# Optimization experiments

Hardware: AMD Instinct MI355X
Metric: run time of the kernel (lower is better)

Reference implementation:

```python
import jax, jax.numpy as jnp
import numpy as np

B, L, D = 8, 2048, 64   # batch, length, input_dim
K, NU = 40, 32          # num scales, reservoir units
LEAKY = 0.0
REG = 1.0


def setup_inputs() -> dict:
    key = jax.random.key(0)
    k1, k2 = jax.random.split(key)
    x = jax.random.normal(k1, (B, L, D), dtype=jnp.float32)
    radii = jax.random.uniform(k2, (K,), dtype=jnp.float32, minval=0.1, maxval=0.99)
    rng = np.random.default_rng(0)
    W_in = jnp.asarray(rng.standard_normal((D, NU)).astype(np.float32))
    # uni_res=True: one sparse reservoir, spectral-radius normalized, repeated K times
    connectivity = min(1.0, 10.0 / NU)
    w = rng.standard_normal((NU, NU)) * (rng.random((NU, NU)) < connectivity)
    w = w / np.max(np.abs(np.linalg.eigvals(w)))
    W_res = jnp.asarray(np.repeat(w[None].astype(np.float32), K, axis=0))
    return {"x": x, "radii": radii, "W_in": W_in, "W_res": W_res}


def reference(x, radii, W_in, W_res):
    Bb, Ll, Dd = x.shape
    k, nu = W_res.shape[0], W_res.shape[1]
    T = Ll - 1
    xt = x @ W_in                                # [B,L,nu]
    Wr = W_res * radii[:, None, None]            # [k,nu,nu]
    ar = jnp.arange(k)

    # Multi-scale recurrence: scale r reads its own state delayed by r+1 steps.
    # Rolling buffer buf[:, r, j] holds column (t-1-j) of scale r's history, so
    # h_pre for scale r is the diagonal buf[:, r, r] (== h_history[:, r, t-r-1];
    # zero for t-r-1 < 0, matching the torch code's untouched zero init).
    def step(buf, x_t):                          # buf [B,k,k,nu], x_t [B,nu]
        h_pre = buf[:, ar, ar, :]                # [B,k,nu] diagonal gather
        h_t = x_t[:, None, :] + jnp.einsum('brn,rnm->brm', h_pre, Wr)
        new = LEAKY * h_pre + (1.0 - LEAKY) * jnp.tanh(h_t)
        buf = jnp.concatenate([new[:, :, None, :], buf[:, :, :-1, :]], axis=2)
        return buf, new

    buf0 = jnp.zeros((Bb, k, k, nu), x.dtype)
    _, hist = jax.lax.scan(step, buf0, jnp.swapaxes(xt[:, :T], 0, 1))
    h_hist = jnp.transpose(hist, (1, 2, 0, 3))   # [B,k,T,nu]

    # Scale i has L-1-i valid timesteps; mask instead of ragged slicing.
    t_idx = jnp.arange(T)
    mask = (t_idx[None, :] < (Ll - 1 - ar)[:, None]).astype(x.dtype)  # [k,T]
    Hm = h_hist * mask[None, :, :, None]          # [B,k,T,nu]
    idx = jnp.minimum(t_idx[None, :] + ar[:, None] + 1, Ll - 1)       # [k,T]
    Xm = x[:, idx, :] * mask[None, :, :, None]    # [B,k,T,D] (x shifted by i+1)

    eye = REG * jnp.eye(nu, dtype=x.dtype)
    HtH = jnp.einsum('bktn,bktm->bknm', Hm, Hm) + eye   # [B,k,nu,nu]
    HtX = jnp.einsum('bktn,bktd->bknd', Hm, Xm)         # [B,k,nu,D]
    W_out = jnp.linalg.solve(HtH, HtX)                  # [B,k,nu,D]

    err = jnp.einsum('bktn,bknd->bktd', Hm, W_out) - Xm
    f_norms = jnp.sum(err, axis=(0, 2, 3))              # [k]
    features = W_out.reshape(Bb, k, nu * Dd)            # [B,k,nu*D]
    return features, f_norms
```

## Files before the change

kernel.cpp:

```cpp
#include <hip/hip_runtime.h>

#define B_ 8
#define L_ 2048
#define D_ 64
#define K_ 40
#define NU_ 32
#define T_ 2047
#define NSPLIT 8

#define XT_OFF   0
#define XT_SZ    (B_*L_*NU_)
#define HH_OFF   (XT_OFF + XT_SZ)
#define HH_SZ    (B_*K_*T_*NU_)
#define HTHP_OFF (HH_OFF + HH_SZ)
#define HTHP_SZ  (NSPLIT*B_*K_*NU_*NU_)
#define HTXP_OFF (HTHP_OFF + HTHP_SZ)
#define HTXP_SZ  (NSPLIT*B_*K_*NU_*D_)
#define SH_OFF   (HTXP_OFF + HTXP_SZ)
#define SH_SZ    (B_*K_*NU_)
#define SX_OFF   (SH_OFF + SH_SZ)
#define SX_SZ    (B_*K_)

#if __has_builtin(__builtin_amdgcn_exp2f)
#define EXP2F(x) __builtin_amdgcn_exp2f(x)
#else
#define EXP2F(x) __expf((x)*0.6931471805599453f)
#endif
#if __has_builtin(__builtin_amdgcn_rcpf)
#define RCPF(x) __builtin_amdgcn_rcpf(x)
#else
#define RCPF(x) (1.0f/(x))
#endif

__global__ __launch_bounds__(256) void k1_xt(const float* __restrict__ x,
                                             const float* __restrict__ Win,
                                             float* __restrict__ xt)
{
    __shared__ float Ws[D_*NU_];
    for (int i = threadIdx.x; i < D_*NU_; i += 256) Ws[i] = Win[i];
    __syncthreads();
    int gid = blockIdx.x*256 + threadIdx.x;
    int m   = gid & 31;
    int row = gid >> 5;
    const float4* xr = (const float4*)(x + (size_t)row * 64);
    float s = 0.f;
#pragma unroll
    for (int q = 0; q < 16; ++q) {
        float4 v = xr[q];
        s = fmaf(v.x, Ws[(q*4+0)*32+m], s);
        s = fmaf(v.y, Ws[(q*4+1)*32+m], s);
        s = fmaf(v.z, Ws[(q*4+2)*32+m], s);
        s = fmaf(v.w, Ws[(q*4+3)*32+m], s);
    }
    xt[gid] = s;
}

__global__ __launch_bounds__(64) void k2_rec(const float* __restrict__ ws_xt,
                                             const float* __restrict__ Wres,
                                             const float* __restrict__ radii,
                                             float* __restrict__ hh)
{
    const int l = threadIdx.x;
    const int m = l & 31;
    int e = blockIdx.x % 820;
    int b = blockIdx.x / 820;
    int r = 0, base = 0;
    while (e >= base + r + 1) { base += r + 1; ++r; }
    const int cc     = e - base;
    const int stride = r + 1;
    const float rad  = radii[r];
    float w[32];
#pragma unroll
    for (int n = 0; n < 32; ++n)
        w[n] = Wres[r*1024 + n*32 + m] * rad;

    const float* xt = ws_xt + (size_t)b * L_ * NU_;
    float* hrow = hh + ((size_t)(b*K_ + r)) * T_ * NU_;

    const int nsteps = (T_ - 1 - cc) / stride + 1;
    const int adv = stride * NU_;
    const float* xp = xt + (size_t)cc * NU_ + m;
    float xv0 = xp[0];
    float xv1 = xp[adv];
    float xv2 = xp[2*adv];
    const float* xp3 = xp + 3*(size_t)adv;
    float* hp = hrow + (size_t)cc * NU_ + l;

    int hb = 0;
#pragma unroll 2
    for (int sstep = 0; sstep < nsteps; ++sstep) {
        float xv3 = *xp3;
        xp3 += adv;
        float a0 = xv0, a1 = 0.f, a2 = 0.f, a3 = 0.f;
#define RL(N, ACC) { int g_ = __builtin_amdgcn_readlane(hb, N); \
                     ACC = fmaf(w[N], __int_as_float(g_), ACC); }
        RL(0,a0)  RL(1,a1)  RL(2,a2)  RL(3,a3)
        RL(4,a0)  RL(5,a1)  RL(6,a2)  RL(7,a3)
        RL(8,a0)  RL(9,a1)  RL(10,a2) RL(11,a3)
        RL(12,a0) RL(13,a1) RL(14,a2) RL(15,a3)
        RL(16,a0) RL(17,a1) RL(18,a2) RL(19,a3)
        RL(20,a0) RL(21,a1) RL(22,a2) RL(23,a3)
        RL(24,a0) RL(25,a1) RL(26,a2) RL(27,a3)
        RL(28,a0) RL(29,a1) RL(30,a2) RL(31,a3)
#undef RL
        float s = (a0 + a1) + (a2 + a3);
        float ex = EXP2F(s * 2.8853900817779268f);
        float hn = fmaf(-2.f, RCPF(ex + 1.f), 1.f);
        if (l < 32) *hp = hn;
        hp += adv;
        hb = __float_as_int(hn);
        xv0 = xv1; xv1 = xv2; xv2 = xv3;
    }
}

__global__ __launch_bounds__(64) void k3_gemm(const float* __restrict__ hh,
                                              const float* __restrict__ x,
                                              float* __restrict__ htHp,
                                              float* __restrict__ htXp,
                                              float* __restrict__ sH,
                                              float* __restrict__ sX)
{
    const int s  = blockIdx.x;
    const int k  = blockIdx.y;
    const int b  = blockIdx.z;
    const int l  = threadIdx.x;
    const int bk = b*K_ + k;
    const int Tk = T_ - k;
    __shared__ __align__(16) float P[32][96];
    const int tidn = l / 12;
    const int tidc = l % 12;

    float acc[8][8];
#pragma unroll
    for (int i = 0; i < 8; ++i)
#pragma unroll
        for (int j = 0; j < 8; ++j) acc[i][j] = 0.f;
    float bsum[8];
#pragma unroll
    for (int j = 0; j < 8; ++j) bsum[j] = 0.f;

    const float* hrow = hh + (size_t)bk * T_ * NU_;
    const float* xrow = x + (size_t)b * L_ * D_ + (size_t)(k+1) * D_;

    for (int ch = s*8; ch < s*8 + 8; ++ch) {
        const int t0 = ch*32;
#pragma unroll
        for (int rd = 0; rd < 12; ++rd) {
            int slot = rd*64 + l;
            int row  = slot / 24;
            int q    = slot % 24;
            int tt   = t0 + row;
            float4 v = make_float4(0.f, 0.f, 0.f, 0.f);
            if (tt < Tk) {
                if (q < 8) v = *(const float4*)(hrow + (size_t)tt*32 + q*4);
                else       v = *(const float4*)(xrow + (size_t)tt*64 + (q-8)*4);
            }
            *(float4*)&P[row][q*4] = v;
        }
        __syncthreads();
        if (l < 48) {
#pragma unroll 4
            for (int tt = 0; tt < 32; ++tt) {
                const float* pr = &P[tt][0];
                float4 A0 = *(const float4*)(pr + tidn*8);
                float4 A1 = *(const float4*)(pr + tidn*8 + 4);
                float4 B0 = *(const float4*)(pr + tidc*8);
                float4 B1 = *(const float4*)(pr + tidc*8 + 4);
                float av[8] = {A0.x,A0.y,A0.z,A0.w,A1.x,A1.y,A1.z,A1.w};
                float bv[8] = {B0.x,B0.y,B0.z,B0.w,B1.x,B1.y,B1.z,B1.w};
#pragma unroll
                for (int i = 0; i < 8; ++i)
#pragma unroll
                    for (int j = 0; j < 8; ++j)
                        acc[i][j] = fmaf(av[i], bv[j], acc[i][j]);
#pragma unroll
                for (int j = 0; j < 8; ++j) bsum[j] += bv[j];
            }
        }
        __syncthreads();
    }
    if (l < 48) {
        const int base_h = (s*(B_*K_) + bk)*NU_*NU_;
        const int base_x = (s*(B_*K_) + bk)*NU_*D_;
#pragma unroll
        for (int i = 0; i < 8; ++i) {
            int n = tidn*8 + i;
#pragma unroll
            for (int j = 0; j < 8; ++j) {
                int c = tidc*8 + j;
                if (c < 32) htHp[base_h + n*32 + c]      = acc[i][j];
                else        htXp[base_x + n*64 + (c-32)] = acc[i][j];
            }
        }
        if (tidn == 0) {
            if (tidc < 4) {
#pragma unroll
                for (int j = 0; j < 8; ++j)
                    atomicAdd(&sH[bk*32 + tidc*8 + j], bsum[j]);
            } else {
                float t = 0.f;
#pragma unroll
                for (int j = 0; j < 8; ++j) t += bsum[j];
                atomicAdd(&sX[bk], t);
            }
        }
    }
}

__global__ __launch_bounds__(64) void k4_solve(const float* __restrict__ htHp,
                                               const float* __restrict__ htXp,
                                               const float* __restrict__ sH,
                                               const float* __restrict__ sX,
                                               float* __restrict__ dout)
{
    const int k  = blockIdx.x;
    const int b  = blockIdx.y;
    const int bk = b*K_ + k;
    const int l  = threadIdx.x;
    __shared__ float As[32][33];
#pragma unroll
    for (int i = 0; i < 16; ++i) {
        int idx = i*64 + l;
        int row = idx >> 5, col = idx & 31;
        float v = (row == col) ? 1.0f : 0.0f;
        for (int s2 = 0; s2 < NSPLIT; ++s2)
            v += htHp[(size_t)(s2*(B_*K_) + bk)*1024 + idx];
        As[row][col] = v;
    }
    __syncthreads();
    for (int j = 0; j < 32; ++j) {
        float d   = sqrtf(As[j][j]);
        float inv = 1.0f / d;
        if (l == j) As[j][j] = d;
        if (l < 32 && l > j) As[l][j] *= inv;
        __syncthreads();
        if (l < 32 && l > j) {
            float lij = As[l][j];
            for (int c = j+1; c <= l; ++c)
                As[l][c] -= lij * As[c][j];
        }
        __syncthreads();
    }
    float y[32];
#pragma unroll
    for (int i = 0; i < 32; ++i) {
        float v = 0.f;
        for (int s2 = 0; s2 < NSPLIT; ++s2)
            v += htXp[(size_t)(s2*(B_*K_) + bk)*2048 + i*64 + l];
        y[i] = v;
    }
#pragma unroll
    for (int i = 0; i < 32; ++i) {
        float v = y[i];
#pragma unroll
        for (int j = 0; j < i; ++j) v = fmaf(-As[i][j], y[j], v);
        y[i] = v / As[i][i];
    }
#pragma unroll
    for (int i = 31; i >= 0; --i) {
        float v = y[i];
#pragma unroll
        for (int j = i+1; j < 32; ++j) v = fmaf(-As[j][i], y[j], v);
        y[i] = v / As[i][i];
    }
    float* fout = dout + (size_t)bk * NU_ * D_;
#pragma unroll
    for (int n = 0; n < 32; ++n) fout[n*64 + l] = y[n];
    const float* sh = sH + bk*32;
    float part = 0.f;
#pragma unroll
    for (int n = 0; n < 32; ++n) part = fmaf(sh[n], y[n], part);
#pragma unroll
    for (int off = 32; off > 0; off >>= 1) part += __shfl_xor(part, off);
    if (l == 0) atomicAdd(dout + (size_t)(B_*K_*NU_*D_) + k, part - sX[bk]);
}

extern "C" void kernel_launch(void* const* d_in, const int* in_sizes, int n_in,
                              void* d_out, int out_size, void* d_ws, size_t ws_size,
                              hipStream_t stream)
{
    const float* x     = (const float*)d_in[0];
    const float* radii = (const float*)d_in[1];
    const float* Win   = (const float*)d_in[2];
    const float* Wres  = (const float*)d_in[3];
    float* ws   = (float*)d_ws;
    float* xt   = ws + XT_OFF;
    float* hh   = ws + HH_OFF;
    float* htHp = ws + HTHP_OFF;
    float* htXp = ws + HTXP_OFF;
    float* sH   = ws + SH_OFF;
    float* sX   = ws + SX_OFF;
    float* out  = (float*)d_out;

    hipMemsetAsync(sH, 0, (size_t)(SH_SZ + SX_SZ)*sizeof(float), stream);
    hipMemsetAsync(out + (size_t)B_*K_*NU_*D_, 0, K_*sizeof(float), stream);

    k1_xt <<<(B_*L_*NU_)/256, 256, 0, stream>>>(x, Win, xt);
    k2_rec<<<B_*820, 64, 0, stream>>>(xt, Wres, radii, hh);
    k3_gemm<<<dim3(NSPLIT, K_, B_), 64, 0, stream>>>(hh, x, htHp, htXp, sH, sX);
    k4_solve<<<dim3(K_, B_), 64, 0, stream>>>(htHp, htXp, sH, sX, out);
}
```

Measured before the change: 1.089 ms.

## Fuse reservoir recurrence with Gram accumulation and drop the history buffer

The recurrence kernel now accumulates H^T H, H^T X and the column sums in registers as each state is produced. Results go to global memory through atomics, so the full hidden-state history is never written and the separate GEMM kernel is removed. Blocks are reordered by scale with hardware priorities favouring the long chains, the cross-lane broadcast switches from readlane to ds_bpermute, and inputs are prefetched in chunks of eight steps. Extra 'ballast' blocks spin on FMAs until the scale-0 chains signal completion, which burns compute on otherwise idle units. The catch is more arithmetic per serial step, and heavy register pressure from 96+ live accumulators.

```diff
diff --git a/kernel.cpp b/kernel.cpp
--- a/kernel.cpp
+++ b/kernel.cpp
@@ -6,20 +6,22 @@
 #define K_ 40
 #define NU_ 32
 #define T_ 2047
-#define NSPLIT 8
+#define NCHAIN 6560
+#define NBALLAST 256
 
 #define XT_OFF   0
 #define XT_SZ    (B_*L_*NU_)
-#define HH_OFF   (XT_OFF + XT_SZ)
-#define HH_SZ    (B_*K_*T_*NU_)
-#define HTHP_OFF (HH_OFF + HH_SZ)
-#define HTHP_SZ  (NSPLIT*B_*K_*NU_*NU_)
-#define HTXP_OFF (HTHP_OFF + HTHP_SZ)
-#define HTXP_SZ  (NSPLIT*B_*K_*NU_*D_)
-#define SH_OFF   (HTXP_OFF + HTXP_SZ)
+#define HTH_OFF  (XT_OFF + XT_SZ)
+#define HTH_SZ   (B_*K_*NU_*NU_)
+#define HTX_OFF  (HTH_OFF + HTH_SZ)
+#define HTX_SZ   (B_*K_*NU_*D_)
+#define SH_OFF   (HTX_OFF + HTX_SZ)
 #define SH_SZ    (B_*K_*NU_)
 #define SX_OFF   (SH_OFF + SH_SZ)
 #define SX_SZ    (B_*K_)
+#define DONE_OFF (SX_OFF + SX_SZ)
+#define DONE_SZ  8
+#define ZERO_SZ  (HTH_SZ + HTX_SZ + SH_SZ + SX_SZ + DONE_SZ)
 
 #if __has_builtin(__builtin_amdgcn_exp2f)
 #define EXP2F(x) __builtin_amdgcn_exp2f(x)
@@ -31,6 +33,10 @@
 #else
 #define RCPF(x) (1.0f/(x))
 #endif
+
+#define R32(F) F(0) F(1) F(2) F(3) F(4) F(5) F(6) F(7) F(8) F(9) F(10) F(11) \
+               F(12) F(13) F(14) F(15) F(16) F(17) F(18) F(19) F(20) F(21) F(22) \
+               F(23) F(24) F(25) F(26) F(27) F(28) F(29) F(30) F(31)
 
 __global__ __launch_bounds__(256) void k1_xt(const float* __restrict__ x,
                                              const float* __restrict__ Win,
@@ -55,160 +61,174 @@
     xt[gid] = s;
 }
 
-__global__ __launch_bounds__(64) void k2_rec(const float* __restrict__ ws_xt,
+#define BPV(N) __int_as_float(__builtin_amdgcn_ds_bpermute(zbase + ((N)<<2), hb))
+
+#define DOA(N, ACC) { float bpv = BPV(N); \
+    ACC    = fmaf(w##N, bpv, ACC); \
+    aH##N  = fmaf(hp,   bpv, aH##N); \
+    aX##N  = fmaf(xlag, bpv, aX##N); }
+
+#define STEP(XTV, XXV) { \
+    float hp = __int_as_float(hb); \
+    float a0 = XTV, a1 = 0.f, a2 = 0.f, a3 = 0.f; \
+    DOA(0,a0)  DOA(1,a1)  DOA(2,a2)  DOA(3,a3) \
+    DOA(4,a0)  DOA(5,a1)  DOA(6,a2)  DOA(7,a3) \
+    DOA(8,a0)  DOA(9,a1)  DOA(10,a2) DOA(11,a3) \
+    DOA(12,a0) DOA(13,a1) DOA(14,a2) DOA(15,a3) \
+    DOA(16,a0) DOA(17,a1) DOA(18,a2) DOA(19,a3) \
+    DOA(20,a0) DOA(21,a1) DOA(22,a2) DOA(23,a3) \
+    DOA(24,a0) DOA(25,a1) DOA(26,a2) DOA(27,a3) \
+    DOA(28,a0) DOA(29,a1) DOA(30,a2) DOA(31,a3) \
+    shacc += hp; sxacc += xlag; \
+    float sdot = (a0 + a1) + (a2 + a3); \
+    float ex = EXP2F(sdot * 2.8853900817779268f); \
+    float hn = fmaf(-2.f, RCPF(ex + 1.f), 1.f); \
+    hb = __float_as_int(hn); \
+    xlag = XXV; }
+
+#define MINT(tt) ((tt) > (L_-1) ? (L_-1) : (tt))
+
+#define STAGE(XT, XX) { \
+    XT##0 = xtb[(size_t)MINT(tstage + 0*st)*NU_]; \
+    XT##1 = xtb[(size_t)MINT(tstage + 1*st)*NU_]; \
+    XT##2 = xtb[(size_t)MINT(tstage + 2*st)*NU_]; \
+    XT##3 = xtb[(size_t)MINT(tstage + 3*st)*NU_]; \
+    XT##4 = xtb[(size_t)MINT(tstage + 4*st)*NU_]; \
+    XT##5 = xtb[(size_t)MINT(tstage + 5*st)*NU_]; \
+    XT##6 = xtb[(size_t)MINT(tstage + 6*st)*NU_]; \
+    XT##7 = xtb[(size_t)MINT(tstage + 7*st)*NU_]; \
+    XX##0 = xcb[(size_t)MINT(tstage + 0*st + roff)*D_]; \
+    XX##1 = xcb[(size_t)MINT(tstage + 1*st + roff)*D_]; \
+    XX##2 = xcb[(size_t)MINT(tstage + 2*st + roff)*D_]; \
+    XX##3 = xcb[(size_t)MINT(tstage + 3*st + roff)*D_]; \
+    XX##4 = xcb[(size_t)MINT(tstage + 4*st + roff)*D_]; \
+    XX##5 = xcb[(size_t)MINT(tstage + 5*st + roff)*D_]; \
+    XX##6 = xcb[(size_t)MINT(tstage + 6*st + roff)*D_]; \
+    XX##7 = xcb[(size_t)MINT(tstage + 7*st + roff)*D_]; \
+    tstage += 8*st; }
+
+#define CHUNK(XTc, XXc, XTn, XXn) { \
+    STAGE(XTn, XXn) \
+    STEP(XTc##0, XXc##0) STEP(XTc##1, XXc##1) STEP(XTc##2, XXc##2) STEP(XTc##3, XXc##3) \
+    STEP(XTc##4, XXc##4) STEP(XTc##5, XXc##5) STEP(XTc##6, XXc##6) STEP(XTc##7, XXc##7) }
+
+#define D8(P) float P##0,P##1,P##2,P##3,P##4,P##5,P##6,P##7;
+
+__global__ __launch_bounds__(64, 2) void k2f(const float* __restrict__ ws_xt,
                                              const float* __restrict__ Wres,
                                              const float* __restrict__ radii,
-                                             float* __restrict__ hh)
+                                             const float* __restrict__ x,
+                                             float* __restrict__ htH,
+                                             float* __restrict__ htX,
+                                             float* __restrict__ sH,
+                                             float* __restrict__ sX,
+                                             int*   __restrict__ done)
 {
     const int l = threadIdx.x;
+
+    if (blockIdx.x >= NCHAIN) {
+        float f0 = (float)l + 1.f, f1 = f0*1.5f, f2 = f0*2.5f, f3 = f0*3.5f;
+        int guard = 1 << 17;
+        while (__hip_atomic_load(done, __ATOMIC_RELAXED,
+                                 __HIP_MEMORY_SCOPE_AGENT) < B_ && --guard) {
+#pragma unroll
+            for (int i = 0; i < 64; ++i) {
+                f0 = fmaf(f0, 1.0000001f, 1e-9f);
+                f1 = fmaf(f1, 1.0000001f, 1e-9f);
+                f2 = fmaf(f2, 1.0000001f, 1e-9f);
+                f3 = fmaf(f3, 1.0000001f, 1e-9f);
+            }
+            asm volatile("" :: "v"(f0), "v"(f1), "v"(f2), "v"(f3));
+        }
+        return;
+    }
+
     const int m = l & 31;
-    int e = blockIdx.x % 820;
-    int b = blockIdx.x / 820;
-    int r = 0, base = 0;
-    while (e >= base + r + 1) { base += r + 1; ++r; }
-    const int cc     = e - base;
-    const int stride = r + 1;
-    const float rad  = radii[r];
-    float w[32];
-#pragma unroll
-    for (int n = 0; n < 32; ++n)
-        w[n] = Wres[r*1024 + n*32 + m] * rad;
-
-    const float* xt = ws_xt + (size_t)b * L_ * NU_;
-    float* hrow = hh + ((size_t)(b*K_ + r)) * T_ * NU_;
-
-    const int nsteps = (T_ - 1 - cc) / stride + 1;
-    const int adv = stride * NU_;
-    const float* xp = xt + (size_t)cc * NU_ + m;
-    float xv0 = xp[0];
-    float xv1 = xp[adv];
-    float xv2 = xp[2*adv];
-    const float* xp3 = xp + 3*(size_t)adv;
-    float* hp = hrow + (size_t)cc * NU_ + l;
-
-    int hb = 0;
-#pragma unroll 2
-    for (int sstep = 0; sstep < nsteps; ++sstep) {
-        float xv3 = *xp3;
-        xp3 += adv;
-        float a0 = xv0, a1 = 0.f, a2 = 0.f, a3 = 0.f;
-#define RL(N, ACC) { int g_ = __builtin_amdgcn_readlane(hb, N); \
-                     ACC = fmaf(w[N], __int_as_float(g_), ACC); }
-        RL(0,a0)  RL(1,a1)  RL(2,a2)  RL(3,a3)
-        RL(4,a0)  RL(5,a1)  RL(6,a2)  RL(7,a3)
-        RL(8,a0)  RL(9,a1)  RL(10,a2) RL(11,a3)
-        RL(12,a0) RL(13,a1) RL(14,a2) RL(15,a3)
-        RL(16,a0) RL(17,a1) RL(18,a2) RL(19,a3)
-        RL(20,a0) RL(21,a1) RL(22,a2) RL(23,a3)
-        RL(24,a0) RL(25,a1) RL(26,a2) RL(27,a3)
-        RL(28,a0) RL(29,a1) RL(30,a2) RL(31,a3)
-#undef RL
-        float s = (a0 + a1) + (a2 + a3);
-        float ex = EXP2F(s * 2.8853900817779268f);
-        float hn = fmaf(-2.f, RCPF(ex + 1.f), 1.f);
-        if (l < 32) *hp = hn;
-        hp += adv;
-        hb = __float_as_int(hn);
-        xv0 = xv1; xv1 = xv2; xv2 = xv3;
+    int g = blockIdx.x;
+    int r = 0, cum = 8;
+    while (g >= cum) { ++r; cum += 8*(r+1); }
+    const int local = g - (cum - 8*(r+1));
+    const int b = local / (r+1);
+    const int c = local % (r+1);
+    const int st   = r + 1;
+    const int roff = r + 1;
+    const float rad = radii[r];
+
+    if (r == 0)      __builtin_amdgcn_s_setprio(3);
+    else if (r <= 2) __builtin_amdgcn_s_setprio(2);
+    else if (r <= 6) __builtin_amdgcn_s_setprio(1);
+
+    const float* Wp = Wres + r*1024 + m;
+    #define DECL_W(N) float w##N = Wp[(N)*NU_] * rad;
+    R32(DECL_W)
+    #define DECL_AH(N) float aH##N = 0.f;
+    R32(DECL_AH)
+    #define DECL_AX(N) float aX##N = 0.f;
+    R32(DECL_AX)
+
+    const float* xtb = ws_xt + (size_t)b * L_ * NU_ + m;
+    const float* xcb = x     + (size_t)b * L_ * D_  + l;
+
+    int zbase = 0;
+    asm volatile("" : "+v"(zbase));
+
+    const int nsteps = (T_ - 1 - r - c) / st + 1;
+    const int nfull  = nsteps >> 3;
+    const int tail   = nsteps & 7;
+
+    D8(ta) D8(tb) D8(xa) D8(xb)
+    int tstage = c;
+    STAGE(ta, xa)
+
+    int   hb    = 0;
+    float xlag  = 0.f;
+    float shacc = 0.f, sxacc = 0.f;
+
+    int c2 = 0;
+    for (; c2 + 2 <= nfull; c2 += 2) {
+        CHUNK(ta, xa, tb, xb)
+        CHUNK(tb, xb, ta, xa)
+    }
+    if (c2 < nfull) { CHUNK(ta, xa, tb, xb) }
+
+    int tcur = c + nfull*8*st;
+    for (int j = 0; j < tail; ++j) {
+        float xtv = xtb[(size_t)tcur * NU_];
+        float xxv = xcb[(size_t)(tcur + roff) * D_];
+        STEP(xtv, xxv)
+        tcur += st;
+    }
+
+    {
+        float hp = __int_as_float(hb);
+        #define FIN(N) { float bpv = BPV(N); \
+            aH##N = fmaf(hp, bpv, aH##N); aX##N = fmaf(xlag, bpv, aX##N); }
+        R32(FIN)
+        shacc += hp; sxacc += xlag;
+    }
+
+    const int bk = b*K_ + r;
+    float* pX = htX + (size_t)bk * (NU_*D_) + l;
+    #define ATX(N) atomicAdd(pX + (N)*D_, aX##N);
+    R32(ATX)
+    if (l < NU_) {
+        float* pH = htH + (size_t)bk * (NU_*NU_) + m;
+        #define ATH(N) atomicAdd(pH + (N)*NU_, aH##N);
+        R32(ATH)
+        atomicAdd(&sH[bk*NU_ + m], shacc);
+    }
+#pragma unroll
+    for (int off = 32; off > 0; off >>= 1) sxacc += __shfl_xor(sxacc, off);
+    if (l == 0) {
+        atomicAdd(&sX[bk], sxacc);
+        if (r == 0)
+            __hip_atomic_fetch_add(done, 1, __ATOMIC_RELAXED,
+                                   __HIP_MEMORY_SCOPE_AGENT);
     }
 }
 
-__global__ __launch_bounds__(64) void k3_gemm(const float* __restrict__ hh,
-                                              const float* __restrict__ x,
-                                              float* __restrict__ htHp,
-                                              float* __restrict__ htXp,
-                                              float* __restrict__ sH,
-                                              float* __restrict__ sX)
-{
-    const int s  = blockIdx.x;
-    const int k  = blockIdx.y;
-    const int b  = blockIdx.z;
-    const int l  = threadIdx.x;
-    const int bk = b*K_ + k;
-    const int Tk = T_ - k;
-    __shared__ __align__(16) float P[32][96];
-    const int tidn = l / 12;
-    const int tidc = l % 12;
-
-    float acc[8][8];
-#pragma unroll
-    for (int i = 0; i < 8; ++i)
-#pragma unroll
-        for (int j = 0; j < 8; ++j) acc[i][j] = 0.f;
-    float bsum[8];
-#pragma unroll
-    for (int j = 0; j < 8; ++j) bsum[j] = 0.f;
-
-    const float* hrow = hh + (size_t)bk * T_ * NU_;
-    const float* xrow = x + (size_t)b * L_ * D_ + (size_t)(k+1) * D_;
-
-    for (int ch = s*8; ch < s*8 + 8; ++ch) {
-        const int t0 = ch*32;
-#pragma unroll
-        for (int rd = 0; rd < 12; ++rd) {
-            int slot = rd*64 + l;
-            int row  = slot / 24;
-            int q    = slot % 24;
-            int tt   = t0 + row;
-            float4 v = make_float4(0.f, 0.f, 0.f, 0.f);
-            if (tt < Tk) {
-                if (q < 8) v = *(const float4*)(hrow + (size_t)tt*32 + q*4);
-                else       v = *(const float4*)(xrow + (size_t)tt*64 + (q-8)*4);
-            }
-            *(float4*)&P[row][q*4] = v;
-        }
-        __syncthreads();
-        if (l < 48) {
-#pragma unroll 4
-            for (int tt = 0; tt < 32; ++tt) {
-                const float* pr = &P[tt][0];
-                float4 A0 = *(const float4*)(pr + tidn*8);
-                float4 A1 = *(const float4*)(pr + tidn*8 + 4);
-                float4 B0 = *(const float4*)(pr + tidc*8);
-                float4 B1 = *(const float4*)(pr + tidc*8 + 4);
-                float av[8] = {A0.x,A0.y,A0.z,A0.w,A1.x,A1.y,A1.z,A1.w};
-                float bv[8] = {B0.x,B0.y,B0.z,B0.w,B1.x,B1.y,B1.z,B1.w};
-#pragma unroll
-                for (int i = 0; i < 8; ++i)
-#pragma unroll
-                    for (int j = 0; j < 8; ++j)
-                        acc[i][j] = fmaf(av[i], bv[j], acc[i][j]);
-#pragma unroll
-                for (int j = 0; j < 8; ++j) bsum[j] += bv[j];
-            }
-        }
-        __syncthreads();
-    }
-    if (l < 48) {
-        const int base_h = (s*(B_*K_) + bk)*NU_*NU_;
-        const int base_x = (s*(B_*K_) + bk)*NU_*D_;
-#pragma unroll
-        for (int i = 0; i < 8; ++i) {
-            int n = tidn*8 + i;
-#pragma unroll
-            for (int j = 0; j < 8; ++j) {
-                int c = tidc*8 + j;
-                if (c < 32) htHp[base_h + n*32 + c]      = acc[i][j];
-                else        htXp[base_x + n*64 + (c-32)] = acc[i][j];
-            }
-        }
-        if (tidn == 0) {
-            if (tidc < 4) {
-#pragma unroll
-                for (int j = 0; j < 8; ++j)
-                    atomicAdd(&sH[bk*32 + tidc*8 + j], bsum[j]);
-            } else {
-                float t = 0.f;
-#pragma unroll
-                for (int j = 0; j < 8; ++j) t += bsum[j];
-                atomicAdd(&sX[bk], t);
-            }
-        }
-    }
-}
-
-__global__ __launch_bounds__(64) void k4_solve(const float* __restrict__ htHp,
-                                               const float* __restrict__ htXp,
+__global__ __launch_bounds__(64) void k4_solve(const float* __restrict__ htH,
+                                               const float* __restrict__ htX,
                                                const float* __restrict__ sH,
                                                const float* __restrict__ sX,
                                                float* __restrict__ dout)
@@ -222,10 +242,7 @@
     for (int i = 0; i < 16; ++i) {
         int idx = i*64 + l;
         int row = idx >> 5, col = idx & 31;
-        float v = (row == col) ? 1.0f : 0.0f;
-        for (int s2 = 0; s2 < NSPLIT; ++s2)
-            v += htHp[(size_t)(s2*(B_*K_) + bk)*1024 + idx];
-        As[row][col] = v;
+        As[row][col] = htH[(size_t)bk*1024 + idx] + ((row == col) ? 1.0f : 0.0f);
     }
     __syncthreads();
     for (int j = 0; j < 32; ++j) {
@@ -243,12 +260,8 @@
     }
     float y[32];
 #pragma unroll
-    for (int i = 0; i < 32; ++i) {
-        float v = 0.f;
-        for (int s2 = 0; s2 < NSPLIT; ++s2)
-            v += htXp[(size_t)(s2*(B_*K_) + bk)*2048 + i*64 + l];
-        y[i] = v;
-    }
+    for (int i = 0; i < 32; ++i)
+        y[i] = htX[(size_t)bk*2048 + i*64 + l];
 #pragma unroll
     for (int i = 0; i < 32; ++i) {
         float v = y[i];
@@ -283,20 +296,20 @@
     const float* radii = (const float*)d_in[1];
     const float* Win   = (const float*)d_in[2];
     const float* Wres  = (const float*)d_in[3];
-    float* ws   = (float*)d_ws;
-    float* xt   = ws + XT_OFF;
-    float* hh   = ws + HH_OFF;
-    float* htHp = ws + HTHP_OFF;
-    float* htXp = ws + HTXP_OFF;
-    float* sH   = ws + SH_OFF;
-    float* sX   = ws + SX_OFF;
-    float* out  = (float*)d_out;
-
-    hipMemsetAsync(sH, 0, (size_t)(SH_SZ + SX_SZ)*sizeof(float), stream);
+    float* ws  = (float*)d_ws;
+    float* xt  = ws + XT_OFF;
+    float* htH = ws + HTH_OFF;
+    float* htX = ws + HTX_OFF;
+    float* sH  = ws + SH_OFF;
+    float* sX  = ws + SX_OFF;
+    int*   done = (int*)(ws + DONE_OFF);
+    float* out = (float*)d_out;
+
+    hipMemsetAsync(htH, 0, (size_t)ZERO_SZ*sizeof(float), stream);
     hipMemsetAsync(out + (size_t)B_*K_*NU_*D_, 0, K_*sizeof(float), stream);
 
-    k1_xt <<<(B_*L_*NU_)/256, 256, 0, stream>>>(x, Win, xt);
-    k2_rec<<<B_*820, 64, 0, stream>>>(xt, Wres, radii, hh);
-    k3_gemm<<<dim3(NSPLIT, K_, B_), 64, 0, stream>>>(hh, x, htHp, htXp, sH, sX);
-    k4_solve<<<dim3(K_, B_), 64, 0, stream>>>(htHp, htXp, sH, sX, out);
+    k1_xt<<<(B_*L_*NU_)/256, 256, 0, stream>>>(x, Win, xt);
+    k2f  <<<NCHAIN + NBALLAST, 64, 0, stream>>>(xt, Wres, radii, x,
+                                                htH, htX, sH, sX, done);
+    k4_solve<<<dim3(K_, B_), 64, 0, stream>>>(htH, htX, sH, sX, out);
 }
```

Measured after the change: 3.323 ms. 3.05x slower.
